# Kernel tuning notes

Hardware: AMD Instinct MI355X
Metric: run time of the kernel (lower is better)

The kernel has to match this reference:

```python
import jax, jax.numpy as jnp
import numpy as np

IMG_H, IMG_W = 1024, 1024
STRIDES = (8, 16, 32, 64, 128)
NUM_CLASSES = 80
CONF_THR = 0.05
IOU_THR = 0.5
MAX_PER_CLASS = 100
MAX_DET = 100
K_CAND = 256  # candidates kept per class before greedy NMS (pre-sort cap)


def build_grids():
    gy, gx, gs = [], [], []
    for s in STRIDES:
        H, W = IMG_H // s, IMG_W // s
        h = jnp.arange(H, dtype=jnp.float32)
        w = jnp.arange(W, dtype=jnp.float32)
        gy_, gx_ = jnp.meshgrid(h, w)  # 'xy' indexing -> shape [W, H], matches tf.meshgrid
        gy.append(gy_.reshape(-1))
        gx.append(gx_.reshape(-1))
        gs.append(jnp.full((W * H,), float(s), dtype=jnp.float32))
    return jnp.concatenate(gy), jnp.concatenate(gx), jnp.concatenate(gs)


def pairwise_iou(b):
    # b: [K,4] as (y1, x1, y2, x2)
    y1, x1, y2, x2 = b[:, 0], b[:, 1], b[:, 2], b[:, 3]
    area = (y2 - y1) * (x2 - x1)
    ih = jnp.maximum(jnp.minimum(y2[:, None], y2[None, :]) - jnp.maximum(y1[:, None], y1[None, :]), 0.0)
    iw = jnp.maximum(jnp.minimum(x2[:, None], x2[None, :]) - jnp.maximum(x1[:, None], x1[None, :]), 0.0)
    inter = ih * iw
    union = area[:, None] + area[None, :] - inter
    return inter / jnp.maximum(union, 1e-8)


def nms_one_class(boxes, scores):
    # boxes [N,4], scores [N] -> (sel_boxes [MAX_PER_CLASS,4], sel_scores [MAX_PER_CLASS])
    top_s, idx = jax.lax.top_k(scores, K_CAND)
    cand = boxes[idx]                       # [K,4]
    valid = top_s > CONF_THR
    iou = jax.lax.stop_gradient(pairwise_iou(cand))  # suppression mask is non-differentiable
    rng = jnp.arange(K_CAND)

    def body(i, keep):
        sup = (iou[i] > IOU_THR) & (rng > i) & keep[i]
        return keep & ~sup

    keep = jax.lax.fori_loop(0, K_CAND, body, valid)
    kept = jnp.where(keep, top_s, 0.0)
    sel_s, sel_i = jax.lax.top_k(kept, MAX_PER_CLASS)
    return cand[sel_i], sel_s


def combined_nms(boxes, scores):
    # per image: boxes [N,4] shared across classes, scores [N,C]
    cls_boxes, cls_scores = jax.vmap(nms_one_class, in_axes=(None, 1))(boxes, scores)
    C = scores.shape[1]
    cls_labels = jnp.broadcast_to(jnp.arange(C, dtype=jnp.float32)[:, None], cls_scores.shape)
    flat_s = cls_scores.reshape(-1)
    flat_b = cls_boxes.reshape(-1, 4)
    flat_l = cls_labels.reshape(-1)
    fin_s, fin_i = jax.lax.top_k(flat_s, MAX_DET)
    fin_b = flat_b[fin_i] * (fin_s > 0.0)[:, None].astype(flat_b.dtype)  # zero pad boxes like TF
    fin_l = flat_l[fin_i]
    return fin_b, fin_l, fin_s


def decode(pred_regs, pred_ctrs, pred_clfs):
    gy, gx, gs = build_grids()
    gy, gx, gs = gy[:, None], gx[:, None], gs[:, None]     # [N,1]
    score = pred_clfs * pred_ctrs                           # [B,N,C]
    x1 = gx - pred_regs[..., 0:1]
    x2 = gx + pred_regs[..., 1:2]
    y1 = gy - pred_regs[..., 2:3]
    y2 = gy + pred_regs[..., 3:4]
    bbox = jnp.concatenate([y1, x1, y2, x2], axis=-1) * gs  # [B,N,4] in image coords
    return jax.vmap(combined_nms)(bbox, score)


def setup_inputs() -> dict:
    key = jax.random.key(0)
    k1, k2, k3 = jax.random.split(key, 3)
    N = sum((IMG_H // s) * (IMG_W // s) for s in STRIDES)  # 21824
    B = 16
    return {
        "pred_regs": jax.random.uniform(k1, (B, N, 4), jnp.float32),
        "pred_ctrs": jax.random.uniform(k2, (B, N, 1), jnp.float32),
        "pred_clfs": jax.random.uniform(k3, (B, N, NUM_CLASSES), jnp.float32),
    }


def reference(pred_regs, pred_ctrs, pred_clfs):
    # returns (final_bboxes [B,100,4], final_labels [B,100] float, final_scores [B,100])
    return decode(pred_regs, pred_ctrs, pred_clfs)
```

## Files before the change

### kernel.cpp

```cpp
#include <hip/hip_runtime.h>
#include <stdint.h>

#pragma clang fp contract(off)

namespace {
constexpr int kN = 21824;
constexpr int kB = 16;
constexpr int kC = 80;
constexpr int kK = 256;
constexpr int kMaxPC = 100;
constexpr int kMaxDet = 100;
constexpr int kBins1 = 2048;
constexpr int kCap = 1536;
constexpr int kQCap = 320;
constexpr int kSortN = 512;
constexpr int kRows = kB * kC;
constexpr int kTiles = kN / 64;
constexpr int kTPB = 6;
constexpr int kGScan = (kTiles + kTPB - 1) / kTPB;
constexpr int kLCap = 48;
constexpr float kThr = 0.72f;
}

__device__ __forceinline__ uint64_t make_key(float s, int n) {
  return ((uint64_t)__float_as_uint(s) << 16) | (uint32_t)(0xFFFF - n);
}

__device__ uint32_t block_scan_incl(uint32_t val) {
  __shared__ uint32_t wsum[4];
  int lane = threadIdx.x & 63;
  int wave = threadIdx.x >> 6;
  for (int d = 1; d < 64; d <<= 1) {
    uint32_t t = __shfl_up(val, (unsigned)d, 64);
    if (lane >= d) val += t;
  }
  if (lane == 63) wsum[wave] = val;
  __syncthreads();
  uint32_t off = 0;
  for (int w = 0; w < wave; ++w) off += wsum[w];
  __syncthreads();
  return val + off;
}

struct RegSrc {
  uint64_t k[6];
  int cnt;
  template <class F> __device__ void each(F f) const {
    #pragma unroll
    for (int j = 0; j < 6; ++j)
      if (j < cnt) f(k[j]);
  }
};
struct ColSrc {
  const float* cl;
  const float* ct;
  template <class F> __device__ void each(F f) const {
    for (int n = threadIdx.x; n < kN; n += 256)
      f(make_key(cl[(size_t)n * kC] * ct[n], n));
  }
};
struct ArrSrc {
  const float* s;
  int count;
  template <class F> __device__ void each(F f) const {
    for (int i = threadIdx.x; i < count; i += 256) f(make_key(s[i], i));
  }
};

template <class Src>
__device__ int refine_gather(const Src& src, int K, int cap,
                             uint32_t* hist, uint64_t* cbuf) {
  __shared__ int sel_bin;
  __shared__ uint32_t sel_hd, sel_above, qcnt;
  int tid = threadIdx.x;

  for (int i = tid; i < kBins1; i += 256) hist[i] = 0;
  __syncthreads();
  src.each([&](uint64_t k) { atomicAdd(&hist[(uint32_t)(k >> 37)], 1u); });
  __syncthreads();
  uint32_t krem = (uint32_t)K;
  {
    uint32_t bl[8], v = 0;
    int base = kBins1 - 1 - 8 * tid;
    for (int j = 0; j < 8; ++j) { bl[j] = hist[base - j]; v += bl[j]; }
    uint32_t S = block_scan_incl(v);
    if (S >= krem && (S - v) < krem) {
      uint32_t cum = S - v;
      for (int j = 0; j < 8; ++j) {
        cum += bl[j];
        if (cum >= krem) { sel_bin = base - j; sel_hd = bl[j]; sel_above = cum - bl[j]; break; }
      }
    }
    __syncthreads();
  }
  uint64_t prefix = (uint64_t)sel_bin;
  krem = (uint32_t)K - sel_above;
  uint32_t Sge = ((uint32_t)K - krem) + sel_hd;
  int shift = 37;
  __syncthreads();

  while (Sge > (uint32_t)cap) {
    int w = (shift > 8) ? 8 : shift;
    int ns = shift - w, bins = 1 << w, hs = shift;
    for (int i = tid; i < bins; i += 256) hist[i] = 0;
    __syncthreads();
    uint64_t pfx = prefix;
    src.each([&](uint64_t k) {
      if ((k >> hs) == pfx)
        atomicAdd(&hist[(uint32_t)(k >> ns) & (bins - 1)], 1u);
    });
    __syncthreads();
    uint32_t v = (tid < bins) ? hist[bins - 1 - tid] : 0;
    uint32_t S = block_scan_incl(v);
    if (v && S >= krem && (S - v) < krem) {
      sel_bin = bins - 1 - tid; sel_hd = v; sel_above = S - v;
    }
    __syncthreads();
    prefix = (prefix << w) | (uint32_t)sel_bin;
    krem -= sel_above;
    Sge = ((uint32_t)K - krem) + sel_hd;
    shift = ns;
    __syncthreads();
  }

  uint64_t L = prefix << shift;
  if (tid == 0) qcnt = 0;
  __syncthreads();
  src.each([&](uint64_t k) {
    if (k >= L) {
      uint32_t p = atomicAdd(&qcnt, 1u);
      if (p < (uint32_t)cap) cbuf[p] = k;
    }
  });
  __syncthreads();
  int Scnt = (int)qcnt;
  return Scnt > cap ? cap : Scnt;
}

__global__ __launch_bounds__(256) void score_scan_kernel(
    const float* __restrict__ clfs, const float* __restrict__ ctrs,
    uint32_t* __restrict__ gcnt, uint64_t* __restrict__ glist) {
  int b = blockIdx.y;
  int t0 = blockIdx.x * kTPB;
  int t1 = t0 + kTPB; if (t1 > kTiles) t1 = kTiles;
  int nbase = t0 * 64;
  int nanch = (t1 - t0) * 64;

  __shared__ uint64_t lbuf[kC][kLCap + 1];
  __shared__ uint32_t lcnt[kC];
  __shared__ uint32_t gbase[kC];
  __shared__ float ct[kTPB * 64];
  int tid = threadIdx.x;
  for (int i = tid; i < kC; i += 256) lcnt[i] = 0;
  for (int i = tid; i < nanch; i += 256) ct[i] = ctrs[(size_t)b * kN + nbase + i];
  __syncthreads();

  const float4* src = (const float4*)(clfs + ((size_t)b * kN + nbase) * kC);
  int n4 = nanch * (kC / 4);
  float4 v = (tid < n4) ? src[tid] : float4{0, 0, 0, 0};
  for (int e = tid; e < n4; e += 256) {
    int en = e + 256;
    float4 vn = (en < n4) ? src[en] : float4{0, 0, 0, 0};
    int a = e / 20;
    int c0 = (e % 20) * 4;
    float cv = ct[a];
    int n = nbase + a;
    float sv[4] = {v.x * cv, v.y * cv, v.z * cv, v.w * cv};
    #pragma unroll
    for (int j = 0; j < 4; ++j) {
      if (sv[j] > kThr) {
        int c = c0 + j;
        uint32_t p = atomicAdd(&lcnt[c], 1u);
        if (p < kLCap) lbuf[c][p] = make_key(sv[j], n);
      }
    }
    v = vn;
  }
  __syncthreads();

  if (tid < kC) {
    uint32_t m = lcnt[tid];
    int row = b * kC + tid;
    if (m > kLCap) {
      atomicAdd(&gcnt[row], (uint32_t)(kCap + 1));
      gbase[tid] = 0xFFFFFFFFu;
    } else {
      gbase[tid] = m ? atomicAdd(&gcnt[row], m) : 0u;
    }
  }
  __syncthreads();

  int lane = tid & 63, wave = tid >> 6;
  for (int c = wave * 20; c < wave * 20 + 20; ++c) {
    uint32_t m = lcnt[c];
    uint32_t base = gbase[c];
    if (base == 0xFFFFFFFFu || m == 0) continue;
    if (m > kLCap) m = kLCap;
    int row = b * kC + c;
    for (uint32_t i = lane; i < m; i += 64) {
      uint32_t p = base + i;
      if (p < kCap) glist[(size_t)row * kCap + p] = lbuf[c][i];
    }
  }
}

__device__ __forceinline__ void iou_row_range(
    const float4& A, float aA, const float4* boxes, const float* areas,
    uint32_t (*sup)[8], int row, int j0, int j1 ) {
  int j = j0;
  while (j < j1) {
    int wend = ((j >> 5) << 5) + 32;
    if (wend > j1) wend = j1;
    int w = j >> 5;
    uint32_t cur = 0, m = 1u << (j & 31);
    for (; j < wend; ++j) {
      const float4 Bx = boxes[j];
      float aB = areas[j];
      float yy1 = fmaxf(A.x, Bx.x);
      float yy2 = fminf(A.z, Bx.z);
      float xx1 = fmaxf(A.y, Bx.y);
      float xx2 = fminf(A.w, Bx.w);
      float ih = fmaxf(yy2 - yy1, 0.0f);
      float iw = fmaxf(xx2 - xx1, 0.0f);
      float inter = ih * iw;
      float un = (aB + aA) - inter;
      float unc = fmaxf(un, 1e-8f);
      cur |= (inter + inter > unc) ? m : 0u;
      m += m;
    }
    if (cur) atomicOr(&sup[row][w], cur);
  }
}

__global__ __launch_bounds__(256) void nms_class_kernel(
    const uint32_t* __restrict__ gcnt, const uint64_t* __restrict__ glist,
    const float* __restrict__ clfs, const float* __restrict__ ctrs,
    const float* __restrict__ regs,
    float* __restrict__ cls_boxes, float* __restrict__ cls_scores) {
  int row = blockIdx.x;
  int b = row / kC, c = row % kC;
  int tid = threadIdx.x;
  int lane = tid & 63, wave = tid >> 6;

  __shared__ union alignas(16) {
    uint32_t hist[kBins1];
    uint64_t sortb[kSortN];
    uint32_t supm[kK][8];
  } hu;
  __shared__ float4 boxf4[kK];
  __shared__ float barea[kK];
  __shared__ uint64_t kinit[4];
  __shared__ uint64_t kfin[4];

  uint32_t cnt = gcnt[row];
  int Scnt;
  if (cnt >= (uint32_t)kK && cnt <= (uint32_t)kCap) {
    RegSrc rs; rs.cnt = 0;
    const uint64_t* gl = glist + (size_t)row * kCap;
    #pragma unroll
    for (int j = 0; j < 6; ++j) {
      int i = tid + j * 256;
      if (i < (int)cnt) { rs.k[j] = gl[i]; rs.cnt = j + 1; }
    }
    Scnt = refine_gather(rs, kK, kSortN, hu.hist, hu.sortb);
  } else {
    ColSrc cs{clfs + (size_t)b * kN * kC + c, ctrs + (size_t)b * kN};
    Scnt = refine_gather(cs, kK, kSortN, hu.hist, hu.sortb);
  }

  for (int i = Scnt + tid; i < kSortN; i += 256) hu.sortb[i] = 0;
  __syncthreads();
  uint64_t e0 = hu.sortb[2 * tid], e1 = hu.sortb[2 * tid + 1];
  #pragma unroll
  for (int k2 = 2; k2 <= kSortN; k2 <<= 1) {
    #pragma unroll
    for (int j = k2 >> 1; j >= 2; j >>= 1) {
      bool up = ((tid & (k2 >> 1)) == 0);
      uint64_t p0, p1;
      bool low;
      if (j >= 128) {
        __syncthreads();
        hu.sortb[2 * tid] = e0; hu.sortb[2 * tid + 1] = e1;
        __syncthreads();
        int pi = (2 * tid) ^ j;
        p0 = hu.sortb[pi]; p1 = hu.sortb[pi + 1];
        low = ((tid & (j >> 1)) == 0);
      } else {
        int d = j >> 1;
        p0 = (uint64_t)__shfl_xor((unsigned long long)e0, d, 64);
        p1 = (uint64_t)__shfl_xor((unsigned long long)e1, d, 64);
        low = ((tid & d) == 0);
      }
      bool keepMax = (up == low);
      e0 = (keepMax == (e0 > p0)) ? e0 : p0;
      e1 = (keepMax == (e1 > p1)) ? e1 : p1;
    }
    {
      bool up = ((tid & (k2 >> 1)) == 0);
      bool sw = up ? (e0 < e1) : (e0 > e1);
      uint64_t t0 = sw ? e1 : e0, t1 = sw ? e0 : e1;
      e0 = t0; e1 = t1;
    }
  }
  __syncthreads();
  hu.sortb[2 * tid] = e0; hu.sortb[2 * tid + 1] = e1;
  __syncthreads();
  uint64_t myk = hu.sortb[tid];
  __syncthreads();

  int n = 0xFFFF - (int)(myk & 0xFFFF);
  float sc_v = __uint_as_float((uint32_t)(myk >> 16));
  int off, hl;
  float sf;
  if (n < 16384)      { off = 0;     hl = 7; sf = 8.f;   }
  else if (n < 20480) { off = 16384; hl = 6; sf = 16.f;  }
  else if (n < 21504) { off = 20480; hl = 5; sf = 32.f;  }
  else if (n < 21760) { off = 21504; hl = 4; sf = 64.f;  }
  else                { off = 21760; hl = 3; sf = 128.f; }
  int kk = n - off;
  float gx = (float)(kk >> hl);
  float gy = (float)(kk & ((1 << hl) - 1));
  const float4 r = ((const float4*)regs)[(size_t)b * kN + n];
  float4 mybox;
  mybox.x = (gy - r.z) * sf;
  mybox.y = (gx - r.x) * sf;
  mybox.z = (gy + r.w) * sf;
  mybox.w = (gx + r.y) * sf;
  float my_a = (mybox.z - mybox.x) * (mybox.w - mybox.y);
  boxf4[tid] = mybox;
  barea[tid] = my_a;
  unsigned long long vm = __ballot(sc_v > 0.05f);
  if (lane == 0) kinit[wave] = vm;
  {
    uint64_t* sp = (uint64_t*)&hu.supm[0][0];
    #pragma unroll
    for (int q = 0; q < 4; ++q) sp[tid + q * 256] = 0;
  }
  __syncthreads();

  if (tid < 128) {
    iou_row_range(mybox, my_a, boxf4, barea, hu.supm, tid, tid + 1, tid + 128);
  } else {
    int T = tid - 128;
    float4 bA = boxf4[T]; float aA = barea[T];
    iou_row_range(bA, aA, boxf4, barea, hu.supm, T, T + 128, 256);
    if (T > 0) {
      int rB = 255 - T;
      float4 bB = boxf4[rB]; float aB = barea[rB];
      iou_row_range(bB, aB, boxf4, barea, hu.supm, rB, 256 - T, 256);
    }
  }
  __syncthreads();

  if (wave == 0) {
    uint64_t kw0 = kinit[0], kw1 = kinit[1], kw2 = kinit[2], kw3 = kinit[3];
    #define NMS_SECTION(W, KW)                                              \
      _Pragma("unroll")                                                     \
      for (int ch = 0; ch < 16; ++ch) {                                     \
        const ulonglong2* s0 = (const ulonglong2*)hu.supm[(W << 6) + ch * 4 + 0]; \
        const ulonglong2* s1 = (const ulonglong2*)hu.supm[(W << 6) + ch * 4 + 1]; \
        const ulonglong2* s2 = (const ulonglong2*)hu.supm[(W << 6) + ch * 4 + 2]; \
        const ulonglong2* s3 = (const ulonglong2*)hu.supm[(W << 6) + ch * 4 + 3]; \
        ulonglong2 aL = s0[0], aH = s0[1];                                  \
        ulonglong2 bL = s1[0], bH = s1[1];                                  \
        ulonglong2 cL = s2[0], cH = s2[1];                                  \
        ulonglong2 dL = s3[0], dH = s3[1];                                  \
        if ((KW >> (ch * 4 + 0)) & 1ull) { kw0 &= ~aL.x; kw1 &= ~aL.y; kw2 &= ~aH.x; kw3 &= ~aH.y; } \
        if ((KW >> (ch * 4 + 1)) & 1ull) { kw0 &= ~bL.x; kw1 &= ~bL.y; kw2 &= ~bH.x; kw3 &= ~bH.y; } \
        if ((KW >> (ch * 4 + 2)) & 1ull) { kw0 &= ~cL.x; kw1 &= ~cL.y; kw2 &= ~cH.x; kw3 &= ~cH.y; } \
        if ((KW >> (ch * 4 + 3)) & 1ull) { kw0 &= ~dL.x; kw1 &= ~dL.y; kw2 &= ~dH.x; kw3 &= ~dH.y; } \
      }
    NMS_SECTION(0, kw0)
    NMS_SECTION(1, kw1)
    NMS_SECTION(2, kw2)
    NMS_SECTION(3, kw3)
    #undef NMS_SECTION
    if (lane == 0) { kfin[0] = kw0; kfin[1] = kw1; kfin[2] = kw2; kfin[3] = kw3; }
  }
  __syncthreads();

  uint64_t kw0 = kfin[0], kw1 = kfin[1], kw2 = kfin[2], kw3 = kfin[3];
  uint64_t ww = (wave == 0) ? kw0 : (wave == 1) ? kw1 : (wave == 2) ? kw2 : kw3;
  bool keptf = (ww >> lane) & 1ull;
  int kept_total = (int)(__popcll(kw0) + __popcll(kw1) +
                         __popcll(kw2) + __popcll(kw3));
  int kept_before = (int)__popcll(ww & ((1ull << lane) - 1ull));
  if (wave > 0) kept_before += (int)__popcll(kw0);
  if (wave > 1) kept_before += (int)__popcll(kw1);
  if (wave > 2) kept_before += (int)__popcll(kw2);

  int rank2 = keptf ? kept_before : (kept_total + tid - kept_before);
  if (rank2 < kMaxPC) {
    float ks = keptf ? sc_v : 0.0f;
    size_t obase = ((size_t)row) * kMaxPC + rank2;
    cls_scores[obase] = ks;
    float* ob = cls_boxes + obase * 4;
    ob[0] = mybox.x; ob[1] = mybox.y; ob[2] = mybox.z; ob[3] = mybox.w;
  }
}

__global__ __launch_bounds__(256) void final_topk_kernel(
    const float* __restrict__ cls_scores, const float* __restrict__ cls_boxes,
    float* __restrict__ out) {
  int b = blockIdx.x;
  int tid = threadIdx.x;
  const int M = kC * kMaxPC;
  __shared__ uint32_t hist[kBins1];
  __shared__ uint64_t cbuf[kQCap];

  ArrSrc as{cls_scores + (size_t)b * M, M};
  int Scnt = refine_gather(as, kMaxDet, kQCap, hist, cbuf);

  for (int j = tid; j < Scnt; j += 256) {
    uint64_t myk = cbuf[j];
    int rank = 0;
    for (int i = 0; i < Scnt; ++i) rank += (cbuf[i] > myk);
    if (rank < kMaxDet) {
      float sv = __uint_as_float((uint32_t)(myk >> 16));
      int f = 0xFFFF - (int)(myk & 0xFFFF);
      int cls = f / 100;
      const float* bp = cls_boxes + ((size_t)b * M + f) * 4;
      float m = (sv > 0.0f) ? 1.0f : 0.0f;
      float* ob = out + ((size_t)b * kMaxDet + rank) * 4;
      ob[0] = bp[0] * m; ob[1] = bp[1] * m; ob[2] = bp[2] * m; ob[3] = bp[3] * m;
      out[(size_t)kB * kMaxDet * 4 + (size_t)b * kMaxDet + rank] = (float)cls;
      out[(size_t)kB * kMaxDet * 5 + (size_t)b * kMaxDet + rank] = sv;
    }
  }
}

extern "C" void kernel_launch(void* const* d_in, const int* in_sizes, int n_in,
                              void* d_out, int out_size, void* d_ws, size_t ws_size,
                              hipStream_t stream) {
  (void)in_sizes; (void)n_in; (void)out_size;
  const float* regs = (const float*)d_in[0];
  const float* ctrs = (const float*)d_in[1];
  const float* clfs = (const float*)d_in[2];
  float* out = (float*)d_out;

  const size_t glB  = (size_t)kRows * kCap * sizeof(uint64_t);
  const size_t cbB  = (size_t)kRows * kMaxPC * 4 * sizeof(float);
  const size_t csB  = (size_t)kRows * kMaxPC * sizeof(float);
  const size_t cntB = 8192;
  if (ws_size < glB + cbB + csB + cntB) return;

  char* p = (char*)d_ws;
  uint64_t* glist   = (uint64_t*)p; p += glB;
  float* cls_boxes  = (float*)p;    p += cbB;
  float* cls_scores = (float*)p;    p += csB;
  uint32_t* gcnt    = (uint32_t*)p;

  hipMemsetAsync(gcnt, 0, (size_t)kRows * sizeof(uint32_t), stream);
  score_scan_kernel<<<dim3(kGScan, kB), 256, 0, stream>>>(clfs, ctrs, gcnt, glist);
  nms_class_kernel<<<kRows, 256, 0, stream>>>(gcnt, glist, clfs, ctrs, regs,
                                              cls_boxes, cls_scores);
  final_topk_kernel<<<kB, 256, 0, stream>>>(cls_scores, cls_boxes, out);
}
```

Measured before the change: 273.5 us.

## Specialize radix select, word-aligned IoU masks, bitonic sort in final top-k

On the fast path, refine_gather now builds its first histogram from key bits 28-38 and assumes the top exponent bits are fixed at 0x3F000, since gathered candidates lie above the score threshold. This skips coarse refinement passes. The IoU suppression loop is rewritten to compute whole 32-bit words with a fixed-trip unrolled loop and edge masks, and the NMS kernel gets a launch_bounds occupancy hint. The final top-k swaps the O(n^2) rank counting for a shared 512-element bitonic sort, at the cost of a larger candidate cap and sort overhead.

```diff
diff --git a/kernel.cpp b/kernel.cpp
--- a/kernel.cpp
+++ b/kernel.cpp
@@ -12,7 +12,6 @@
 constexpr int kMaxDet = 100;
 constexpr int kBins1 = 2048;
 constexpr int kCap = 1536;
-constexpr int kQCap = 320;
 constexpr int kSortN = 512;
 constexpr int kRows = kB * kC;
 constexpr int kTiles = kN / 64;
@@ -67,7 +66,7 @@
   }
 };
 
-template <class Src>
+template <class Src, bool FAST>
 __device__ int refine_gather(const Src& src, int K, int cap,
                              uint32_t* hist, uint64_t* cbuf) {
   __shared__ int sel_bin;
@@ -76,7 +75,10 @@
 
   for (int i = tid; i < kBins1; i += 256) hist[i] = 0;
   __syncthreads();
-  src.each([&](uint64_t k) { atomicAdd(&hist[(uint32_t)(k >> 37)], 1u); });
+  src.each([&](uint64_t k) {
+    uint32_t bin = FAST ? (uint32_t)((k >> 28) & 0x7FF) : (uint32_t)(k >> 37);
+    atomicAdd(&hist[bin], 1u);
+  });
   __syncthreads();
   uint32_t krem = (uint32_t)K;
   {
@@ -93,10 +95,11 @@
     }
     __syncthreads();
   }
-  uint64_t prefix = (uint64_t)sel_bin;
+  uint64_t prefix = FAST ? (uint64_t)(0x3F000u | (uint32_t)sel_bin)
+                         : (uint64_t)sel_bin;
+  int shift = FAST ? 28 : 37;
   krem = (uint32_t)K - sel_above;
   uint32_t Sge = ((uint32_t)K - krem) + sel_hd;
-  int shift = 37;
   __syncthreads();
 
   while (Sge > (uint32_t)cap) {
@@ -135,6 +138,45 @@
   __syncthreads();
   int Scnt = (int)qcnt;
   return Scnt > cap ? cap : Scnt;
+}
+
+__device__ __forceinline__ void bitonic512_desc(uint64_t* sortb) {
+  int tid = threadIdx.x;
+  uint64_t e0 = sortb[2 * tid], e1 = sortb[2 * tid + 1];
+  #pragma unroll
+  for (int k2 = 2; k2 <= kSortN; k2 <<= 1) {
+    #pragma unroll
+    for (int j = k2 >> 1; j >= 2; j >>= 1) {
+      bool up = ((tid & (k2 >> 1)) == 0);
+      uint64_t p0, p1;
+      bool low;
+      if (j >= 128) {
+        __syncthreads();
+        sortb[2 * tid] = e0; sortb[2 * tid + 1] = e1;
+        __syncthreads();
+        int pi = (2 * tid) ^ j;
+        p0 = sortb[pi]; p1 = sortb[pi + 1];
+        low = ((tid & (j >> 1)) == 0);
+      } else {
+        int d = j >> 1;
+        p0 = (uint64_t)__shfl_xor((unsigned long long)e0, d, 64);
+        p1 = (uint64_t)__shfl_xor((unsigned long long)e1, d, 64);
+        low = ((tid & d) == 0);
+      }
+      bool keepMax = (up == low);
+      e0 = (keepMax == (e0 > p0)) ? e0 : p0;
+      e1 = (keepMax == (e1 > p1)) ? e1 : p1;
+    }
+    {
+      bool up = ((tid & (k2 >> 1)) == 0);
+      bool sw = up ? (e0 < e1) : (e0 > e1);
+      uint64_t t0 = sw ? e1 : e0, t1 = sw ? e0 : e1;
+      e0 = t0; e1 = t1;
+    }
+  }
+  __syncthreads();
+  sortb[2 * tid] = e0; sortb[2 * tid + 1] = e1;
+  __syncthreads();
 }
 
 __global__ __launch_bounds__(256) void score_scan_kernel(
@@ -204,35 +246,44 @@
   }
 }
 
-__device__ __forceinline__ void iou_row_range(
+__device__ __forceinline__ uint32_t iou_word32(
     const float4& A, float aA, const float4* boxes, const float* areas,
-    uint32_t (*sup)[8], int row, int j0, int j1 ) {
-  int j = j0;
-  while (j < j1) {
-    int wend = ((j >> 5) << 5) + 32;
-    if (wend > j1) wend = j1;
-    int w = j >> 5;
-    uint32_t cur = 0, m = 1u << (j & 31);
-    for (; j < wend; ++j) {
-      const float4 Bx = boxes[j];
-      float aB = areas[j];
-      float yy1 = fmaxf(A.x, Bx.x);
-      float yy2 = fminf(A.z, Bx.z);
-      float xx1 = fmaxf(A.y, Bx.y);
-      float xx2 = fminf(A.w, Bx.w);
-      float ih = fmaxf(yy2 - yy1, 0.0f);
-      float iw = fmaxf(xx2 - xx1, 0.0f);
-      float inter = ih * iw;
-      float un = (aB + aA) - inter;
-      float unc = fmaxf(un, 1e-8f);
-      cur |= (inter + inter > unc) ? m : 0u;
-      m += m;
-    }
+    uint32_t mask) {
+  uint32_t cur = 0;
+  #pragma unroll 8
+  for (int s = 31; s >= 0; --s) {
+    const float4 Bx = boxes[s];
+    float aB = areas[s];
+    float yy1 = fmaxf(A.x, Bx.x);
+    float yy2 = fminf(A.z, Bx.z);
+    float xx1 = fmaxf(A.y, Bx.y);
+    float xx2 = fminf(A.w, Bx.w);
+    float ih = fmaxf(yy2 - yy1, 0.0f);
+    float iw = fmaxf(xx2 - xx1, 0.0f);
+    float inter = ih * iw;
+    float un = (aB + aA) - inter;
+    float unc = fmaxf(un, 1e-8f);
+    cur = (cur << 1) | (uint32_t)(inter + inter > unc);
+  }
+  return cur & mask;
+}
+
+__device__ __forceinline__ void iou_row_words(
+    const float4& A, float aA, const float4* boxes, const float* areas,
+    uint32_t (*sup)[8], int row, int lo, int hi ) {
+  int w0 = lo >> 5, w1 = (hi - 1) >> 5;
+  uint32_t mb = 0xFFFFFFFFu << (lo & 31);
+  uint32_t me = (hi & 31) ? ((1u << (hi & 31)) - 1u) : 0xFFFFFFFFu;
+  for (int w = w0; w <= w1; ++w) {
+    uint32_t mask = 0xFFFFFFFFu;
+    if (w == w0) mask &= mb;
+    if (w == w1) mask &= me;
+    uint32_t cur = iou_word32(A, aA, boxes + (w << 5), areas + (w << 5), mask);
     if (cur) atomicOr(&sup[row][w], cur);
   }
 }
 
-__global__ __launch_bounds__(256) void nms_class_kernel(
+__global__ __launch_bounds__(256, 5) void nms_class_kernel(
     const uint32_t* __restrict__ gcnt, const uint64_t* __restrict__ glist,
     const float* __restrict__ clfs, const float* __restrict__ ctrs,
     const float* __restrict__ regs,
@@ -262,49 +313,15 @@
       int i = tid + j * 256;
       if (i < (int)cnt) { rs.k[j] = gl[i]; rs.cnt = j + 1; }
     }
-    Scnt = refine_gather(rs, kK, kSortN, hu.hist, hu.sortb);
+    Scnt = refine_gather<RegSrc, true>(rs, kK, kSortN, hu.hist, hu.sortb);
   } else {
     ColSrc cs{clfs + (size_t)b * kN * kC + c, ctrs + (size_t)b * kN};
-    Scnt = refine_gather(cs, kK, kSortN, hu.hist, hu.sortb);
+    Scnt = refine_gather<ColSrc, false>(cs, kK, kSortN, hu.hist, hu.sortb);
   }
 
   for (int i = Scnt + tid; i < kSortN; i += 256) hu.sortb[i] = 0;
   __syncthreads();
-  uint64_t e0 = hu.sortb[2 * tid], e1 = hu.sortb[2 * tid + 1];
-  #pragma unroll
-  for (int k2 = 2; k2 <= kSortN; k2 <<= 1) {
-    #pragma unroll
-    for (int j = k2 >> 1; j >= 2; j >>= 1) {
-      bool up = ((tid & (k2 >> 1)) == 0);
-      uint64_t p0, p1;
-      bool low;
-      if (j >= 128) {
-        __syncthreads();
-        hu.sortb[2 * tid] = e0; hu.sortb[2 * tid + 1] = e1;
-        __syncthreads();
-        int pi = (2 * tid) ^ j;
-        p0 = hu.sortb[pi]; p1 = hu.sortb[pi + 1];
-        low = ((tid & (j >> 1)) == 0);
-      } else {
-        int d = j >> 1;
-        p0 = (uint64_t)__shfl_xor((unsigned long long)e0, d, 64);
-        p1 = (uint64_t)__shfl_xor((unsigned long long)e1, d, 64);
-        low = ((tid & d) == 0);
-      }
-      bool keepMax = (up == low);
-      e0 = (keepMax == (e0 > p0)) ? e0 : p0;
-      e1 = (keepMax == (e1 > p1)) ? e1 : p1;
-    }
-    {
-      bool up = ((tid & (k2 >> 1)) == 0);
-      bool sw = up ? (e0 < e1) : (e0 > e1);
-      uint64_t t0 = sw ? e1 : e0, t1 = sw ? e0 : e1;
-      e0 = t0; e1 = t1;
-    }
-  }
-  __syncthreads();
-  hu.sortb[2 * tid] = e0; hu.sortb[2 * tid + 1] = e1;
-  __syncthreads();
+  bitonic512_desc(hu.sortb);
   uint64_t myk = hu.sortb[tid];
   __syncthreads();
 
@@ -339,15 +356,15 @@
   __syncthreads();
 
   if (tid < 128) {
-    iou_row_range(mybox, my_a, boxf4, barea, hu.supm, tid, tid + 1, tid + 128);
+    iou_row_words(mybox, my_a, boxf4, barea, hu.supm, tid, tid + 1, tid + 128);
   } else {
     int T = tid - 128;
     float4 bA = boxf4[T]; float aA = barea[T];
-    iou_row_range(bA, aA, boxf4, barea, hu.supm, T, T + 128, 256);
+    iou_row_words(bA, aA, boxf4, barea, hu.supm, T, T + 128, 256);
     if (T > 0) {
       int rB = 255 - T;
       float4 bB = boxf4[rB]; float aB = barea[rB];
-      iou_row_range(bB, aB, boxf4, barea, hu.supm, rB, 256 - T, 256);
+      iou_row_words(bB, aB, boxf4, barea, hu.supm, rB, 256 - T, 256);
     }
   }
   __syncthreads();
@@ -405,27 +422,29 @@
   int b = blockIdx.x;
   int tid = threadIdx.x;
   const int M = kC * kMaxPC;
-  __shared__ uint32_t hist[kBins1];
-  __shared__ uint64_t cbuf[kQCap];
+  __shared__ union alignas(16) {
+    uint32_t hist[kBins1];
+    uint64_t sortb[kSortN];
+  } hu;
 
   ArrSrc as{cls_scores + (size_t)b * M, M};
-  int Scnt = refine_gather(as, kMaxDet, kQCap, hist, cbuf);
-
-  for (int j = tid; j < Scnt; j += 256) {
-    uint64_t myk = cbuf[j];
-    int rank = 0;
-    for (int i = 0; i < Scnt; ++i) rank += (cbuf[i] > myk);
-    if (rank < kMaxDet) {
-      float sv = __uint_as_float((uint32_t)(myk >> 16));
-      int f = 0xFFFF - (int)(myk & 0xFFFF);
-      int cls = f / 100;
-      const float* bp = cls_boxes + ((size_t)b * M + f) * 4;
-      float m = (sv > 0.0f) ? 1.0f : 0.0f;
-      float* ob = out + ((size_t)b * kMaxDet + rank) * 4;
-      ob[0] = bp[0] * m; ob[1] = bp[1] * m; ob[2] = bp[2] * m; ob[3] = bp[3] * m;
-      out[(size_t)kB * kMaxDet * 4 + (size_t)b * kMaxDet + rank] = (float)cls;
-      out[(size_t)kB * kMaxDet * 5 + (size_t)b * kMaxDet + rank] = sv;
-    }
+  int Scnt = refine_gather<ArrSrc, false>(as, kMaxDet, kSortN, hu.hist, hu.sortb);
+
+  for (int i = Scnt + tid; i < kSortN; i += 256) hu.sortb[i] = 0;
+  __syncthreads();
+  bitonic512_desc(hu.sortb);
+
+  if (tid < kMaxDet) {
+    uint64_t myk = hu.sortb[tid];
+    float sv = __uint_as_float((uint32_t)(myk >> 16));
+    int f = 0xFFFF - (int)(myk & 0xFFFF);
+    int cls = f / 100;
+    const float* bp = cls_boxes + ((size_t)b * M + f) * 4;
+    float m = (sv > 0.0f) ? 1.0f : 0.0f;
+    float* ob = out + ((size_t)b * kMaxDet + tid) * 4;
+    ob[0] = bp[0] * m; ob[1] = bp[1] * m; ob[2] = bp[2] * m; ob[3] = bp[3] * m;
+    out[(size_t)kB * kMaxDet * 4 + (size_t)b * kMaxDet + tid] = (float)cls;
+    out[(size_t)kB * kMaxDet * 5 + (size_t)b * kMaxDet + tid] = sv;
   }
 }
 
```

Result: no change. 269.3 us (-1.5%).
